# Optimization experiments

Hardware: AMD Instinct MI355X
Metric: run time of the kernel (lower is better)

## Reference

```python
import jax, jax.numpy as jnp
import numpy as np

NUM_HEADS = 16
HEAD_DIM = 64
HIDDEN = NUM_HEADS * HEAD_DIM  # 1024
SEQ_LEN = 4096


def setup_inputs() -> dict:
    key = jax.random.key(0)
    ks = jax.random.split(key, 8)
    hidden_states = jax.random.normal(ks[0], (SEQ_LEN, HIDDEN), dtype=jnp.float32)
    cu_seqlens = jnp.sort(jax.random.randint(ks[1], (5,), 0, SEQ_LEN)).astype(jnp.int32)
    cos = jax.random.uniform(ks[2], (SEQ_LEN, HEAD_DIM), dtype=jnp.float32)
    sin = jax.random.uniform(ks[3], (SEQ_LEN, HEAD_DIM), dtype=jnp.float32)
    W_qkv = jax.random.normal(ks[4], (HIDDEN, 3 * HIDDEN), dtype=jnp.float32) * 0.02
    b_qkv = jax.random.normal(ks[5], (3 * HIDDEN,), dtype=jnp.float32) * 0.02
    W_proj = jax.random.normal(ks[6], (HIDDEN, HIDDEN), dtype=jnp.float32) * 0.02
    b_proj = jax.random.normal(ks[7], (HIDDEN,), dtype=jnp.float32) * 0.02
    return {
        "hidden_states": hidden_states,
        "cu_seqlens": cu_seqlens,
        "cos": cos,
        "sin": sin,
        "W_qkv": W_qkv,
        "b_qkv": b_qkv,
        "W_proj": W_proj,
        "b_proj": b_proj,
    }


def _rotate_half(x):
    x1, x2 = jnp.split(x, 2, axis=-1)
    return jnp.concatenate([-x2, x1], axis=-1)


def reference(hidden_states, cu_seqlens, cos, sin, W_qkv, b_qkv, W_proj, b_proj):
    # NOTE: original module does not use cu_seqlens for masking (full dense attention).
    seq_len = hidden_states.shape[0]
    qkv = hidden_states @ W_qkv + b_qkv  # (S, 3*H)
    qkv = qkv.reshape(seq_len, 3, NUM_HEADS, HEAD_DIM)
    q, k, v = qkv[:, 0], qkv[:, 1], qkv[:, 2]  # (S, nh, hd)
    c = cos[:, None, :]
    s = sin[:, None, :]
    q = q * c + _rotate_half(q) * s
    k = k * c + _rotate_half(k) * s
    scale = 1.0 / jnp.sqrt(jnp.float32(HEAD_DIM))
    # (nh, S, hd)
    q = q.transpose(1, 0, 2)
    k = k.transpose(1, 0, 2)
    v = v.transpose(1, 0, 2)
    attn = jnp.einsum('hqd,hkd->hqk', q, k) * scale
    attn = jax.nn.softmax(attn, axis=-1)
    out = jnp.einsum('hqk,hkd->hqd', attn, v)
    out = out.transpose(1, 0, 2).reshape(seq_len, HIDDEN)
    return out @ W_proj + b_proj
```

## Files before the change

### kernel.cpp

```cpp
#include <hip/hip_runtime.h>
#include <type_traits>

typedef short bf16x8 __attribute__((ext_vector_type(8)));
typedef float f32x4  __attribute__((ext_vector_type(4)));
typedef unsigned short u16;

#define MFMA(a,b,c) __builtin_amdgcn_mfma_f32_16x16x32_bf16((a),(b),(c),0,0,0)

__device__ __forceinline__ float bf2f(u16 u){ unsigned x=((unsigned)u)<<16; return __builtin_bit_cast(float,x); }
__device__ __forceinline__ u16 f2bf(float f){ unsigned x=__builtin_bit_cast(unsigned,f); x += 0x7fffu + ((x>>16)&1u); return (u16)(x>>16); }

#if __has_builtin(__builtin_amdgcn_cvt_pk_bf16_f32)
typedef __bf16 hwbf2 __attribute__((ext_vector_type(2)));
__device__ __forceinline__ unsigned pkbf(float a, float b){
  hwbf2 r = __builtin_amdgcn_cvt_pk_bf16_f32(a, b);
  return __builtin_bit_cast(unsigned, r);
}
#else
__device__ __forceinline__ unsigned pkbf(float a, float b){
  unsigned ua = __builtin_bit_cast(unsigned, a), ub = __builtin_bit_cast(unsigned, b);
  ua += 0x7fffu + ((ua>>16)&1u);
  ub += 0x7fffu + ((ub>>16)&1u);
  return __builtin_amdgcn_perm(ub, ua, 0x07060302u);
}
#endif

#if __has_builtin(__builtin_amdgcn_exp2f)
#define EXP2(x) __builtin_amdgcn_exp2f(x)
#else
#define EXP2(x) exp2f(x)
#endif

__device__ __forceinline__ void async_cp16(const u16* g, u16* l){
  __builtin_amdgcn_global_load_lds((const __attribute__((address_space(1))) void*)g,
                                   (__attribute__((address_space(3))) void*)l, 16, 0, 0);
}

__global__ __launch_bounds__(256) void prep(
    const float* __restrict__ H, const float* __restrict__ Wqkv, const float* __restrict__ Wproj,
    u16* __restrict__ Hb, u16* __restrict__ WqkvT, u16* __restrict__ WprojT)
{
  __shared__ u16 tile[32][33];
  const int bid = blockIdx.x, tid = threadIdx.x;
  if (bid < 4096) {
    int i = (bid*256 + tid)*4;
    float4 v = *(const float4*)(H + i);
    ushort4 o;
    o.x = f2bf(v.x); o.y = f2bf(v.y); o.z = f2bf(v.z); o.w = f2bf(v.w);
    *(ushort4*)(Hb + i) = o;
    return;
  }
  const float* in; u16* out; int R, C, bx, by;
  if (bid < 7168) { int t = bid-4096; in=Wqkv; out=WqkvT; R=1024; C=3072; bx=t%96; by=t/96; }
  else            { int t = bid-7168; in=Wproj; out=WprojT; R=1024; C=1024; bx=t%32; by=t/32; }
  int bc = bx*32, br = by*32;
  int tx = tid & 31, ty = tid >> 5;
  #pragma unroll
  for (int i=ty;i<32;i+=8) tile[i][tx] = f2bf(in[(size_t)(br+i)*C + bc + tx]);
  __syncthreads();
  #pragma unroll
  for (int i=ty;i<32;i+=8) out[(size_t)(bc+i)*R + br + tx] = tile[tx][i];
}

__global__ __launch_bounds__(256) void gemm_qkv_rope(
    const u16* __restrict__ A, const u16* __restrict__ Bt,
    const float* __restrict__ bias, const float* __restrict__ cosb, const float* __restrict__ sinb,
    u16* __restrict__ Qo, u16* __restrict__ Ko, u16* __restrict__ Vt)
{
  constexpr int K = 1024;
  __shared__ __align__(16) u16 smem[128*128];
  u16* const As = smem;
  u16* const Bs = smem + 128*64;
  const int m0 = blockIdx.y*128, n0 = blockIdx.x*128;
  const int tid = threadIdx.x, wave = tid>>6, lane = tid&63;
  const int wr = (wave>>1)*64, wc = (wave&1)*64;
  const int ml = lane&15, quad = lane>>4;
  const int lrow8 = lane>>3, lchk = lane&7;
  const int swzg = (lchk ^ lrow8)*8;
  const u16* gA[4]; u16* lA[4];
  const u16* gB[4]; u16* lB[4];
  #pragma unroll
  for (int t=0;t<4;t++){
    gA[t] = A  + (size_t)(m0 + wave*32 + t*8 + lrow8)*K + swzg;
    lA[t] = &As[(wave*32 + t*8)*64];
    gB[t] = Bt + (size_t)(n0 + wave*32 + t*8 + lrow8)*K + swzg;
    lB[t] = &Bs[(wave*32 + t*8)*64];
  }
  f32x4 acc[4][4] = {};
  const int rch0 = ( quad     ^ (ml&7))*8;
  const int rch1 = ((quad|4) ^ (ml&7))*8;
  for (int k0=0; k0<K; k0+=64) {
    #pragma unroll
    for (int t=0;t<4;t++){ async_cp16(gA[t]+k0, lA[t]); async_cp16(gB[t]+k0, lB[t]); }
    __syncthreads();
    #pragma unroll
    for (int kk=0;kk<2;kk++){
      const int rc = kk ? rch1 : rch0;
      bf16x8 af[4], bfr[4];
      #pragma unroll
      for (int i=0;i<4;i++)  af[i]  = *(const bf16x8*)&As[(wr+i*16+ml)*64 + rc];
      #pragma unroll
      for (int j=0;j<4;j++) bfr[j] = *(const bf16x8*)&Bs[(wc+j*16+ml)*64 + rc];
      #pragma unroll
      for (int i=0;i<4;i++)
        #pragma unroll
        for (int j=0;j<4;j++)
          acc[i][j] = MFMA(af[i], bfr[j], acc[i][j]);
    }
    __syncthreads();
  }
  const int region = n0 >> 10;
  if (region == 2) {
    #pragma unroll
    for (int j=0;j<4;j++){
      int d2 = wc + j*16 + ml;
      float bv = bias[n0 + d2];
      #pragma unroll
      for (int i=0;i<4;i++){
        int t0 = wr + i*16 + quad*4;
        #pragma unroll
        for (int r=0;r<4;r++){
          int t = t0 + r;
          int c = (d2 >> 3) ^ (t & 15);
          smem[t*128 + c*8 + (d2 & 7)] = f2bf(acc[i][j][r] + bv);
        }
      }
    }
    __syncthreads();
    const int hbase = (n0 - 2048) >> 6;
    const int tx = tid & 31, ty = tid >> 5;
    const int tlog32 = ((tx>>2)&1)*16 + (tx>>3)*4 + (tx&3);
    #pragma unroll
    for (int ii=0; ii<16; ii++){
      int d2 = ty + ii*8;
      int hh = hbase + (d2 >> 6);
      int dd = d2 & 63;
      u16* vrow = Vt + ((size_t)hh*64 + dd)*4096 + m0;
      #pragma unroll
      for (int tq=0; tq<4; tq++){
        int t_src = tq*32 + tlog32;
        int c = (d2 >> 3) ^ (t_src & 15);
        vrow[tq*32 + tx] = smem[t_src*128 + c*8 + (d2 & 7)];
      }
    }
  } else {
    u16* dst = region ? Ko : Qo;
    const float qs = region ? 1.0f : 0.125f*1.44269504f;
    #pragma unroll
    for (int j=0;j<4;j++){
      int col = n0 + wc + j*16 + ml;
      int dloc = col & 63, hh = (col & 1023) >> 6;
      float bv  = bias[col];
      float bvp = bias[col ^ 32];
      float sgn = (dloc < 32) ? -1.f : 1.f;
      #pragma unroll
      for (int i=0;i<4;i++){
        int row0 = m0 + wr + i*16 + quad*4;
        #pragma unroll
        for (int r=0;r<4;r++){
          int t = row0 + r;
          float c = cosb[t*64 + dloc], s = sinb[t*64 + dloc];
          float val = acc[i][j][r]   + bv;
          float par = acc[i][j^2][r] + bvp;
          dst[((size_t)hh*4096 + t)*64 + dloc] = f2bf((val*c + sgn*par*s)*qs);
        }
      }
    }
  }
}

template<int BN, typename OutT>
__global__ __launch_bounds__(256) void gemm_bt_bias(
    const u16* __restrict__ A, const u16* __restrict__ Bt,
    const float* __restrict__ bias, OutT* __restrict__ C,
    int M, int N, int K)
{
  __shared__ __align__(16) u16 As[128*64];
  __shared__ __align__(16) u16 Bs[BN*64];
  const int m0 = blockIdx.y*128, n0 = blockIdx.x*BN;
  const int tid = threadIdx.x, wave = tid>>6, lane = tid&63;
  const int wr = (wave>>1)*64, wc = (wave&1)*(BN/2);
  const int ml = lane&15, quad = lane>>4;
  const int lrow8 = lane>>3, lchk = lane&7;
  const int swzg = (lchk ^ lrow8)*8;
  const u16* gA[4]; u16* lA[4];
  #pragma unroll
  for (int t=0;t<4;t++){
    gA[t] = A + (size_t)(m0 + wave*32 + t*8 + lrow8)*K + swzg;
    lA[t] = &As[(wave*32 + t*8)*64];
  }
  constexpr int BI = BN/32;
  const u16* gB[BI]; u16* lB[BI];
  #pragma unroll
  for (int t=0;t<BI;t++){
    gB[t] = Bt + (size_t)(n0 + wave*(BN/4) + t*8 + lrow8)*K + swzg;
    lB[t] = &Bs[(wave*(BN/4) + t*8)*64];
  }
  constexpr int NJ = BN/32;
  f32x4 acc[4][NJ] = {};
  const int rch0 = ( quad     ^ (ml&7))*8;
  const int rch1 = ((quad|4) ^ (ml&7))*8;
  for (int k0=0; k0<K; k0+=64) {
    #pragma unroll
    for (int t=0;t<4;t++)  async_cp16(gA[t]+k0, lA[t]);
    #pragma unroll
    for (int t=0;t<BI;t++) async_cp16(gB[t]+k0, lB[t]);
    __syncthreads();
    #pragma unroll
    for (int kk=0;kk<2;kk++){
      const int rc = kk ? rch1 : rch0;
      bf16x8 af[4], bfr[NJ];
      #pragma unroll
      for (int i=0;i<4;i++)  af[i]  = *(const bf16x8*)&As[(wr+i*16+ml)*64 + rc];
      #pragma unroll
      for (int j=0;j<NJ;j++) bfr[j] = *(const bf16x8*)&Bs[(wc+j*16+ml)*64 + rc];
      #pragma unroll
      for (int i=0;i<4;i++)
        #pragma unroll
        for (int j=0;j<NJ;j++)
          acc[i][j] = MFMA(af[i], bfr[j], acc[i][j]);
    }
    __syncthreads();
  }
  #pragma unroll
  for (int j=0;j<NJ;j++){
    int col = n0 + wc + j*16 + ml;
    float bv = bias[col];
    #pragma unroll
    for (int i=0;i<4;i++){
      int row0 = m0 + wr + i*16 + quad*4;
      #pragma unroll
      for (int r=0;r<4;r++){
        float val = acc[i][j][r] + bv;
        if constexpr (std::is_same_v<OutT, float>)
          C[(size_t)(row0+r)*N + col] = val;
        else
          C[(size_t)(row0+r)*N + col] = f2bf(val);
      }
    }
  }
}

__global__ __launch_bounds__(256,4) void flash_attn(
    const u16* __restrict__ Q, const u16* __restrict__ Kg, const u16* __restrict__ VT,
    u16* __restrict__ O0, u16* __restrict__ O1, u16* __restrict__ O2, u16* __restrict__ O3,
    float* __restrict__ Lpart)
{
  constexpr int SEQ=4096, QTR=1024;
  __shared__ __align__(16) u16 Ks[64*64];
  __shared__ __align__(16) u16 Vs[64*64];
  const int lin = blockIdx.x;
  const int idx = (lin & 7)*256 + (lin >> 3);
  const int qt = idx & 31, h = (idx >> 5) & 15, ks = idx >> 9;
  const int tid=threadIdx.x, wave=tid>>6, lane=tid&63;
  const int ml=lane&15, quad=lane>>4;
  const int qbase = qt*128 + wave*32;
  bf16x8 qf[2][2];
  #pragma unroll
  for (int qi=0; qi<2; qi++){
    const u16* qp = Q + ((size_t)h*SEQ + qbase + qi*16 + ml)*64;
    qf[qi][0] = *(const bf16x8*)(qp + quad*8);
    qf[qi][1] = *(const bf16x8*)(qp + 32 + quad*8);
  }
  const bf16x8 ones = {0x3F80,0x3F80,0x3F80,0x3F80,0x3F80,0x3F80,0x3F80,0x3F80};
  f32x4 o[2][4] = {};
  f32x4 accsum[2] = {};
  const int lrow8 = lane>>3, lchk = lane&7;
  const int swzg = (lchk ^ lrow8)*8;
  const u16* kgl = Kg + (size_t)h*SEQ*64 + (size_t)(ks*QTR + wave*16 + lrow8)*64 + swzg;
  const u16* vgl = VT + (size_t)h*64*SEQ + (size_t)(wave*16 + lrow8)*SEQ + ks*QTR + swzg;
  u16* kl0 = &Ks[(wave*16  )*64];
  u16* kl1 = &Ks[(wave*16+8)*64];
  u16* vl0 = &Vs[(wave*16  )*64];
  u16* vl1 = &Vs[(wave*16+8)*64];
  const int swzA = ( quad     ^ (ml&7))*8;
  const int swzB = ((quad^4) ^ (ml&7))*8;

  for (int k0=0;k0<QTR;k0+=64) {
    async_cp16(kgl + (size_t)k0*64,       kl0);
    async_cp16(kgl + (size_t)k0*64 + 512, kl1);
    async_cp16(vgl + k0,                  vl0);
    async_cp16(vgl + 8*SEQ + k0,          vl1);
    __syncthreads();
    f32x4 s[2][4];
    #pragma unroll
    for (int kb=0;kb<4;kb++){
      bf16x8 kf0 = *(const bf16x8*)&Ks[(kb*16+ml)*64 + swzA];
      bf16x8 kf1 = *(const bf16x8*)&Ks[(kb*16+ml)*64 + swzB];
      f32x4 z0={0,0,0,0}, z1={0,0,0,0};
      z0 = MFMA(kf0, qf[0][0], z0); s[0][kb] = MFMA(kf1, qf[0][1], z0);
      z1 = MFMA(kf0, qf[1][0], z1); s[1][kb] = MFMA(kf1, qf[1][1], z1);
    }
    bf16x8 vf[4][2];
    #pragma unroll
    for (int db=0;db<4;db++){
      vf[db][0] = *(const bf16x8*)&Vs[(db*16+ml)*64 + swzA];
      vf[db][1] = *(const bf16x8*)&Vs[(db*16+ml)*64 + swzB];
    }
    #pragma unroll
    for (int qi=0; qi<2; qi++)
      #pragma unroll
      for (int p=0;p<2;p++){
        float e0 = EXP2(s[qi][2*p][0]),   e1 = EXP2(s[qi][2*p][1]);
        float e2 = EXP2(s[qi][2*p][2]),   e3 = EXP2(s[qi][2*p][3]);
        float e4 = EXP2(s[qi][2*p+1][0]), e5 = EXP2(s[qi][2*p+1][1]);
        float e6 = EXP2(s[qi][2*p+1][2]), e7 = EXP2(s[qi][2*p+1][3]);
        union { uint4 u; bf16x8 v; } pf;
        pf.u.x = pkbf(e0,e1); pf.u.y = pkbf(e2,e3);
        pf.u.z = pkbf(e4,e5); pf.u.w = pkbf(e6,e7);
        accsum[qi] = MFMA(ones, pf.v, accsum[qi]);
        #pragma unroll
        for (int db=0;db<4;db++)
          o[qi][db] = MFMA(vf[db][p], pf.v, o[qi][db]);
      }
    __syncthreads();
  }
  u16* op = (ks==0) ? O0 : (ks==1) ? O1 : (ks==2) ? O2 : O3;
  #pragma unroll
  for (int qi=0;qi<2;qi++){
    size_t rb = (size_t)(qbase + qi*16 + ml)*1024 + h*64;
    #pragma unroll
    for (int db=0;db<4;db++){
      uint2 w;
      w.x = pkbf(o[qi][db][0], o[qi][db][1]);
      w.y = pkbf(o[qi][db][2], o[qi][db][3]);
      *(uint2*)&op[rb + db*16 + quad*4] = w;
    }
  }
  if (quad==0){
    float* lp = Lpart + (size_t)ks*65536 + (size_t)h*4096 + qbase;
    lp[ml]    = accsum[0][0];
    lp[16+ml] = accsum[1][0];
  }
}

__global__ __launch_bounds__(256) void combine_softmax4(
    const u16* __restrict__ O0, const u16* __restrict__ O1,
    const u16* __restrict__ O2, const u16* __restrict__ O3,
    const float* __restrict__ L, u16* __restrict__ AO)
{
  int i = (blockIdx.x*256 + threadIdx.x)*4;
  int row = i >> 10, col = i & 1023, h = col >> 6;
  int li = h*4096 + row;
  float inv = 1.f/(L[li] + L[li+65536] + L[li+2*65536] + L[li+3*65536]);
  ushort4 a = *(const ushort4*)(O0+i);
  ushort4 b = *(const ushort4*)(O1+i);
  ushort4 c = *(const ushort4*)(O2+i);
  ushort4 d = *(const ushort4*)(O3+i);
  ushort4 o;
  o.x = f2bf((bf2f(a.x)+bf2f(b.x)+bf2f(c.x)+bf2f(d.x))*inv);
  o.y = f2bf((bf2f(a.y)+bf2f(b.y)+bf2f(c.y)+bf2f(d.y))*inv);
  o.z = f2bf((bf2f(a.z)+bf2f(b.z)+bf2f(c.z)+bf2f(d.z))*inv);
  o.w = f2bf((bf2f(a.w)+bf2f(b.w)+bf2f(c.w)+bf2f(d.w))*inv);
  *(ushort4*)(AO+i) = o;
}

extern "C" void kernel_launch(void* const* d_in, const int* in_sizes, int n_in,
                              void* d_out, int out_size, void* d_ws, size_t ws_size,
                              hipStream_t stream)
{
  (void)in_sizes; (void)n_in; (void)out_size; (void)ws_size;
  const float* H     = (const float*)d_in[0];
  const float* cosb  = (const float*)d_in[2];
  const float* sinb  = (const float*)d_in[3];
  const float* Wqkv  = (const float*)d_in[4];
  const float* bqkv  = (const float*)d_in[5];
  const float* Wproj = (const float*)d_in[6];
  const float* bproj = (const float*)d_in[7];
  float* out = (float*)d_out;
  char* ws = (char*)d_ws;
  float* Lpart  = (float*)(ws + 0);
  u16*   WprojT = (u16*)(ws + 2097152);
  u16*   Hb     = (u16*)(ws + 4194304);
  u16*   Opart3 = (u16*)(ws + 4194304);
  u16*   Qb     = (u16*)(ws + 12582912);
  u16*   AO     = (u16*)(ws + 12582912);
  u16*   Kb     = (u16*)(ws + 20971520);
  u16*   VTb    = (u16*)(ws + 29360128);
  u16*   WqkvT  = (u16*)(ws + 37748736);
  u16*   Opart0 = (u16*)(ws + 37748736);
  u16*   Opart1 = (u16*)(ws + 46137344);
  u16*   Opart2 = (u16*)(ws + 54525952);

  hipLaunchKernelGGL(prep, dim3(8192), dim3(256), 0, stream, H, Wqkv, Wproj, Hb, WqkvT, WprojT);
  hipLaunchKernelGGL(gemm_qkv_rope, dim3(24,32), dim3(256), 0, stream,
                     Hb, WqkvT, bqkv, cosb, sinb, Qb, Kb, VTb);
  hipLaunchKernelGGL(flash_attn, dim3(2048), dim3(256), 0, stream, Qb, Kb, VTb,
                     Opart0, Opart1, Opart2, Opart3, Lpart);
  hipLaunchKernelGGL(combine_softmax4, dim3(4096), dim3(256), 0, stream,
                     Opart0, Opart1, Opart2, Opart3, Lpart, AO);
  hipLaunchKernelGGL((gemm_bt_bias<64,float>), dim3(16,32), dim3(256), 0, stream,
                     AO, WprojT, bproj, out, 4096, 1024, 1024);
}
```

Baseline: 245.5 us.

## Drop split-K attention and fuse softmax normalization into flash kernel

The attention kernel no longer splits the key sequence into four quarters. Each block now processes all 4096 keys for 64 queries (16 per wave) and divides by the row sum before writing bf16 output directly. This removes the combine kernel, the four partial-output buffers and the partial-sum buffer, along with their global memory traffic and one launch. In exchange each K/V tile loaded into shared memory is reused by half as many queries, the grid shrinks to 1024 blocks, and each block runs a loop four times longer.

```diff
diff --git a/kernel.cpp b/kernel.cpp
--- a/kernel.cpp
+++ b/kernel.cpp
@@ -243,32 +243,30 @@
 
 __global__ __launch_bounds__(256,4) void flash_attn(
     const u16* __restrict__ Q, const u16* __restrict__ Kg, const u16* __restrict__ VT,
-    u16* __restrict__ O0, u16* __restrict__ O1, u16* __restrict__ O2, u16* __restrict__ O3,
-    float* __restrict__ Lpart)
-{
-  constexpr int SEQ=4096, QTR=1024;
+    u16* __restrict__ AO)
+{
+  constexpr int SEQ=4096;
   __shared__ __align__(16) u16 Ks[64*64];
   __shared__ __align__(16) u16 Vs[64*64];
   const int lin = blockIdx.x;
-  const int idx = (lin & 7)*256 + (lin >> 3);
-  const int qt = idx & 31, h = (idx >> 5) & 15, ks = idx >> 9;
+  const int idx = (lin & 7)*128 + (lin >> 3);
+  const int qt = idx & 63, h = idx >> 6;
   const int tid=threadIdx.x, wave=tid>>6, lane=tid&63;
   const int ml=lane&15, quad=lane>>4;
-  const int qbase = qt*128 + wave*32;
-  bf16x8 qf[2][2];
-  #pragma unroll
-  for (int qi=0; qi<2; qi++){
-    const u16* qp = Q + ((size_t)h*SEQ + qbase + qi*16 + ml)*64;
-    qf[qi][0] = *(const bf16x8*)(qp + quad*8);
-    qf[qi][1] = *(const bf16x8*)(qp + 32 + quad*8);
+  const int qbase = qt*64 + wave*16;
+  bf16x8 qf[2];
+  {
+    const u16* qp = Q + ((size_t)h*SEQ + qbase + ml)*64;
+    qf[0] = *(const bf16x8*)(qp + quad*8);
+    qf[1] = *(const bf16x8*)(qp + 32 + quad*8);
   }
   const bf16x8 ones = {0x3F80,0x3F80,0x3F80,0x3F80,0x3F80,0x3F80,0x3F80,0x3F80};
-  f32x4 o[2][4] = {};
-  f32x4 accsum[2] = {};
+  f32x4 o[4] = {};
+  f32x4 accsum = {};
   const int lrow8 = lane>>3, lchk = lane&7;
   const int swzg = (lchk ^ lrow8)*8;
-  const u16* kgl = Kg + (size_t)h*SEQ*64 + (size_t)(ks*QTR + wave*16 + lrow8)*64 + swzg;
-  const u16* vgl = VT + (size_t)h*64*SEQ + (size_t)(wave*16 + lrow8)*SEQ + ks*QTR + swzg;
+  const u16* kgl = Kg + (size_t)h*SEQ*64 + (size_t)(wave*16 + lrow8)*64 + swzg;
+  const u16* vgl = VT + (size_t)h*64*SEQ + (size_t)(wave*16 + lrow8)*SEQ + swzg;
   u16* kl0 = &Ks[(wave*16  )*64];
   u16* kl1 = &Ks[(wave*16+8)*64];
   u16* vl0 = &Vs[(wave*16  )*64];
@@ -276,20 +274,20 @@
   const int swzA = ( quad     ^ (ml&7))*8;
   const int swzB = ((quad^4) ^ (ml&7))*8;
 
-  for (int k0=0;k0<QTR;k0+=64) {
+  for (int k0=0;k0<SEQ;k0+=64) {
     async_cp16(kgl + (size_t)k0*64,       kl0);
     async_cp16(kgl + (size_t)k0*64 + 512, kl1);
     async_cp16(vgl + k0,                  vl0);
     async_cp16(vgl + 8*SEQ + k0,          vl1);
     __syncthreads();
-    f32x4 s[2][4];
+    f32x4 s[4];
     #pragma unroll
     for (int kb=0;kb<4;kb++){
       bf16x8 kf0 = *(const bf16x8*)&Ks[(kb*16+ml)*64 + swzA];
       bf16x8 kf1 = *(const bf16x8*)&Ks[(kb*16+ml)*64 + swzB];
-      f32x4 z0={0,0,0,0}, z1={0,0,0,0};
-      z0 = MFMA(kf0, qf[0][0], z0); s[0][kb] = MFMA(kf1, qf[0][1], z0);
-      z1 = MFMA(kf0, qf[1][0], z1); s[1][kb] = MFMA(kf1, qf[1][1], z1);
+      f32x4 z0={0,0,0,0};
+      z0 = MFMA(kf0, qf[0], z0);
+      s[kb] = MFMA(kf1, qf[1], z0);
     }
     bf16x8 vf[4][2];
     #pragma unroll
@@ -298,61 +296,30 @@
       vf[db][1] = *(const bf16x8*)&Vs[(db*16+ml)*64 + swzB];
     }
     #pragma unroll
-    for (int qi=0; qi<2; qi++)
-      #pragma unroll
-      for (int p=0;p<2;p++){
-        float e0 = EXP2(s[qi][2*p][0]),   e1 = EXP2(s[qi][2*p][1]);
-        float e2 = EXP2(s[qi][2*p][2]),   e3 = EXP2(s[qi][2*p][3]);
-        float e4 = EXP2(s[qi][2*p+1][0]), e5 = EXP2(s[qi][2*p+1][1]);
-        float e6 = EXP2(s[qi][2*p+1][2]), e7 = EXP2(s[qi][2*p+1][3]);
-        union { uint4 u; bf16x8 v; } pf;
-        pf.u.x = pkbf(e0,e1); pf.u.y = pkbf(e2,e3);
-        pf.u.z = pkbf(e4,e5); pf.u.w = pkbf(e6,e7);
-        accsum[qi] = MFMA(ones, pf.v, accsum[qi]);
-        #pragma unroll
-        for (int db=0;db<4;db++)
-          o[qi][db] = MFMA(vf[db][p], pf.v, o[qi][db]);
-      }
-    __syncthreads();
-  }
-  u16* op = (ks==0) ? O0 : (ks==1) ? O1 : (ks==2) ? O2 : O3;
-  #pragma unroll
-  for (int qi=0;qi<2;qi++){
-    size_t rb = (size_t)(qbase + qi*16 + ml)*1024 + h*64;
-    #pragma unroll
-    for (int db=0;db<4;db++){
-      uint2 w;
-      w.x = pkbf(o[qi][db][0], o[qi][db][1]);
-      w.y = pkbf(o[qi][db][2], o[qi][db][3]);
-      *(uint2*)&op[rb + db*16 + quad*4] = w;
-    }
-  }
-  if (quad==0){
-    float* lp = Lpart + (size_t)ks*65536 + (size_t)h*4096 + qbase;
-    lp[ml]    = accsum[0][0];
-    lp[16+ml] = accsum[1][0];
-  }
-}
-
-__global__ __launch_bounds__(256) void combine_softmax4(
-    const u16* __restrict__ O0, const u16* __restrict__ O1,
-    const u16* __restrict__ O2, const u16* __restrict__ O3,
-    const float* __restrict__ L, u16* __restrict__ AO)
-{
-  int i = (blockIdx.x*256 + threadIdx.x)*4;
-  int row = i >> 10, col = i & 1023, h = col >> 6;
-  int li = h*4096 + row;
-  float inv = 1.f/(L[li] + L[li+65536] + L[li+2*65536] + L[li+3*65536]);
-  ushort4 a = *(const ushort4*)(O0+i);
-  ushort4 b = *(const ushort4*)(O1+i);
-  ushort4 c = *(const ushort4*)(O2+i);
-  ushort4 d = *(const ushort4*)(O3+i);
-  ushort4 o;
-  o.x = f2bf((bf2f(a.x)+bf2f(b.x)+bf2f(c.x)+bf2f(d.x))*inv);
-  o.y = f2bf((bf2f(a.y)+bf2f(b.y)+bf2f(c.y)+bf2f(d.y))*inv);
-  o.z = f2bf((bf2f(a.z)+bf2f(b.z)+bf2f(c.z)+bf2f(d.z))*inv);
-  o.w = f2bf((bf2f(a.w)+bf2f(b.w)+bf2f(c.w)+bf2f(d.w))*inv);
-  *(ushort4*)(AO+i) = o;
+    for (int p=0;p<2;p++){
+      float e0 = EXP2(s[2*p][0]),   e1 = EXP2(s[2*p][1]);
+      float e2 = EXP2(s[2*p][2]),   e3 = EXP2(s[2*p][3]);
+      float e4 = EXP2(s[2*p+1][0]), e5 = EXP2(s[2*p+1][1]);
+      float e6 = EXP2(s[2*p+1][2]), e7 = EXP2(s[2*p+1][3]);
+      union { uint4 u; bf16x8 v; } pf;
+      pf.u.x = pkbf(e0,e1); pf.u.y = pkbf(e2,e3);
+      pf.u.z = pkbf(e4,e5); pf.u.w = pkbf(e6,e7);
+      accsum = MFMA(ones, pf.v, accsum);
+      #pragma unroll
+      for (int db=0;db<4;db++)
+        o[db] = MFMA(vf[db][p], pf.v, o[db]);
+    }
+    __syncthreads();
+  }
+  const float inv = 1.0f / accsum[0];
+  size_t rb = (size_t)(qbase + ml)*1024 + h*64;
+  #pragma unroll
+  for (int db=0;db<4;db++){
+    uint2 w;
+    w.x = pkbf(o[db][0]*inv, o[db][1]*inv);
+    w.y = pkbf(o[db][2]*inv, o[db][3]*inv);
+    *(uint2*)&AO[rb + db*16 + quad*4] = w;
+  }
 }
 
 extern "C" void kernel_launch(void* const* d_in, const int* in_sizes, int n_in,
@@ -369,26 +336,18 @@
   const float* bproj = (const float*)d_in[7];
   float* out = (float*)d_out;
   char* ws = (char*)d_ws;
-  float* Lpart  = (float*)(ws + 0);
-  u16*   WprojT = (u16*)(ws + 2097152);
-  u16*   Hb     = (u16*)(ws + 4194304);
-  u16*   Opart3 = (u16*)(ws + 4194304);
-  u16*   Qb     = (u16*)(ws + 12582912);
-  u16*   AO     = (u16*)(ws + 12582912);
-  u16*   Kb     = (u16*)(ws + 20971520);
-  u16*   VTb    = (u16*)(ws + 29360128);
-  u16*   WqkvT  = (u16*)(ws + 37748736);
-  u16*   Opart0 = (u16*)(ws + 37748736);
-  u16*   Opart1 = (u16*)(ws + 46137344);
-  u16*   Opart2 = (u16*)(ws + 54525952);
+  u16*   WprojT = (u16*)(ws + 0);
+  u16*   Hb     = (u16*)(ws + 2097152);
+  u16*   Qb     = (u16*)(ws + 10485760);
+  u16*   Kb     = (u16*)(ws + 18874368);
+  u16*   VTb    = (u16*)(ws + 27262976);
+  u16*   WqkvT  = (u16*)(ws + 35651584);
+  u16*   AO     = (u16*)(ws + 41943040);
 
   hipLaunchKernelGGL(prep, dim3(8192), dim3(256), 0, stream, H, Wqkv, Wproj, Hb, WqkvT, WprojT);
   hipLaunchKernelGGL(gemm_qkv_rope, dim3(24,32), dim3(256), 0, stream,
                      Hb, WqkvT, bqkv, cosb, sinb, Qb, Kb, VTb);
-  hipLaunchKernelGGL(flash_attn, dim3(2048), dim3(256), 0, stream, Qb, Kb, VTb,
-                     Opart0, Opart1, Opart2, Opart3, Lpart);
-  hipLaunchKernelGGL(combine_softmax4, dim3(4096), dim3(256), 0, stream,
-                     Opart0, Opart1, Opart2, Opart3, Lpart, AO);
+  hipLaunchKernelGGL(flash_attn, dim3(1024), dim3(256), 0, stream, Qb, Kb, VTb, AO);
   hipLaunchKernelGGL((gemm_bt_bias<64,float>), dim3(16,32), dim3(256), 0, stream,
                      AO, WprojT, bproj, out, 4096, 1024, 1024);
 }
```

After: 243.7 us. Within noise of the previous version (-0.7%).
